# Kernel tuning notes

Measured on AMD Instinct MI355X. Metric: run time of the kernel, lower is better.

## Reference

```python
import jax, jax.numpy as jnp
import numpy as np

SCALE = 0.125  # (dim // heads) ** -0.5 = (256 // 4) ** -0.5


def setup_inputs() -> dict:
    key = jax.random.key(0)
    k1, k2, k3, k4, k5 = jax.random.split(key, 5)
    dim, red = 256, 4
    c = dim // red  # 64
    B, H, W = 4, 64, 64
    x = jax.random.normal(k1, (B, dim, H, W), dtype=jnp.float32)
    qkv_w = jax.random.normal(k2, (3 * c, dim), dtype=jnp.float32) * 0.02
    qkv_b = jax.random.normal(k3, (3 * c,), dtype=jnp.float32) * 0.02
    proj_w = jax.random.normal(k4, (dim, c), dtype=jnp.float32) * 0.02
    proj_b = jax.random.normal(k5, (dim,), dtype=jnp.float32) * 0.02
    return {"x": x, "qkv_w": qkv_w, "qkv_b": qkv_b, "proj_w": proj_w, "proj_b": proj_b}


def reference(x, qkv_w, qkv_b, proj_w, proj_b):
    B, C, H, W = x.shape
    # 1x1 conv == channel matmul
    qkv = jnp.einsum('bchw,oc->bohw', x, qkv_w) + qkv_b[None, :, None, None]
    c = qkv.shape[1] // 3
    qkv = qkv.reshape(B, 3 * c, H * W)
    q, k, v = qkv[:, :c], qkv[:, c:2 * c], qkv[:, 2 * c:]  # [B, c, HW]
    # attn[b, n, m] = sum_c q[b,c,n] * k[b,c,m] * scale
    attn = jnp.einsum('bcn,bcm->bnm', q, k) * SCALE
    attn = jax.nn.softmax(attn, axis=-1)  # [B, HW, HW]
    # out[b, c, n] = sum_m v[b,c,m] * attn[b,n,m]   (v @ attn^T)
    out = jnp.einsum('bcm,bnm->bcn', v, attn).reshape(B, c, H, W)
    # proj 1x1 conv back to dim
    return jnp.einsum('bchw,oc->bohw', out, proj_w) + proj_b[None, :, None, None]
```

## Files before the change

### kernel.cpp

```cpp
#include <hip/hip_runtime.h>
#include <hip/hip_bf16.h>


#define N_TOK 4096
#define CDIM  64
#define DIM   256
#define NBAT  4

typedef __attribute__((ext_vector_type(8)))  short          short8;
typedef __attribute__((ext_vector_type(8)))  unsigned short ushort8_t;
typedef __attribute__((ext_vector_type(4)))  unsigned short ushort4_t;
typedef __attribute__((ext_vector_type(4)))  unsigned int   uint4_t;
typedef __attribute__((ext_vector_type(4)))  float          float4_t;
typedef __attribute__((ext_vector_type(16))) float          float16_t;

#if __has_builtin(__builtin_amdgcn_exp2f)
#define QSC  0.18033688011112042f
#define PEXP(x) __builtin_amdgcn_exp2f(x)
#else
#define QSC  0.125f
#define PEXP(x) __expf(x)
#endif

__device__ __forceinline__ unsigned short f2bf(float f) {
  unsigned int u = __builtin_bit_cast(unsigned int, f);
  u += 0x7fffu + ((u >> 16) & 1u);
  return (unsigned short)(u >> 16);
}

__device__ __forceinline__ unsigned int pkcv(float a, float b) {
  __hip_bfloat162 h = __float22bfloat162_rn(make_float2(a, b));
  unsigned int r; __builtin_memcpy(&r, &h, 4); return r;
}

__device__ __forceinline__ short8 ld8(const unsigned short* p) {
  return __builtin_bit_cast(short8, *(const ushort8_t*)p);
}

__device__ __forceinline__ short8 pack8f(float4_t a, float4_t b) {
  uint4_t u;
  u[0] = pkcv(a[0], a[1]); u[1] = pkcv(a[2], a[3]);
  u[2] = pkcv(b[0], b[1]); u[3] = pkcv(b[2], b[3]);
  return __builtin_bit_cast(short8, u);
}

__device__ __forceinline__ float16_t z16() {
  float16_t r;
#pragma unroll
  for (int i = 0; i < 16; ++i) r[i] = 0.0f;
  return r;
}

typedef __attribute__((address_space(1))) const void* gvp;
typedef __attribute__((address_space(3))) void*       lvp;
__device__ __forceinline__ void dma16(const unsigned short* g, unsigned short* l) {
  __builtin_amdgcn_global_load_lds((gvp)g, (lvp)l, 16, 0, 0);
}

#define MFMA(a, b, c) __builtin_amdgcn_mfma_f32_32x32x16_bf16((a), (b), (c), 0, 0, 0)

#define QOFF  0
#define KOFF  1048576
#define VOFF  2097152
#define WQOFF 3145728
#define BSOFF 3194880

__global__ void k_prep(const float* __restrict__ qw, const float* __restrict__ qb,
                       unsigned short* __restrict__ wqs, float* __restrict__ bs)
{
  const int g = blockIdx.x * 256 + threadIdx.x;
  {
    const int lane = g & 63, grp = g >> 6;
    const int w6 = grp >> 4, kk = grp & 15;
    const int o = w6 * 32 + (lane & 31);
    const int c = kk * 16 + (lane >> 5) * 8;
    const float sc = (o < 64) ? QSC : 1.0f;
    const float* src = qw + o * 256 + c;
    ushort8_t u;
#pragma unroll
    for (int j = 0; j < 8; ++j) u[j] = f2bf(src[j] * sc);
    *(ushort8_t*)(wqs + g * 8) = u;
  }
  if (g < 48) {
    float4_t f = *(const float4_t*)(qb + g * 4);
    float4_t o;
#pragma unroll
    for (int j = 0; j < 4; ++j) o[j] = f[j] * ((g * 4 + j) < 64 ? QSC : 1.0f);
    *(float4_t*)(bs + g * 4) = o;
  }
}

#define RS 132

__global__ __launch_bounds__(768, 3) void k_qkv(
    const float* __restrict__ x, const unsigned short* __restrict__ wqs,
    const float* __restrict__ bs, unsigned short* __restrict__ Qf,
    unsigned short* __restrict__ Kf, unsigned short* __restrict__ Vf)
{
  __shared__ unsigned int Xl[64 * RS];
  const int id = blockIdx.x;
  const int b  = (id >> 1) & 3;
  const int nt = (id & 1) | ((id >> 3) << 1);
  const int t  = threadIdx.x;
  const int n0g = nt * 64;

  if (t < 512) {
    const int n0  = (t & 15) * 4;
    const int cpb = t >> 4;
#pragma unroll
    for (int p = 0; p < 4; ++p) {
      const int cp = cpb + 32 * p, c = cp * 2;
      const float* xb = x + (((size_t)(b * DIM + c)) << 12) + n0g + n0;
      float4_t a = *(const float4_t*)xb;
      float4_t d = *(const float4_t*)(xb + 4096);
#pragma unroll
      for (int j = 0; j < 4; ++j)
        Xl[(n0 + j) * RS + cp] = pkcv(a[j], d[j]);
    }
  }

  const int w = t >> 6, lane = t & 63, l31 = lane & 31, lh = lane >> 5;
  const int ot = w >> 1, sub = w & 1;
  const int ch = nt * 2 + sub;

  const unsigned short* wrow = wqs + ((ot * 16) << 9) + lane * 8;
  short8 wf[16];
#pragma unroll
  for (int kk = 0; kk < 16; ++kk) wf[kk] = ld8(wrow + (kk << 9));

  __syncthreads();

  const unsigned int* xr = &Xl[(sub * 32 + l31) * RS + lh * 4];

  float16_t a0 = z16();
  if (ot < 4) {
#pragma unroll
    for (int kk = 0; kk < 16; ++kk) {
      short8 xf = __builtin_bit_cast(short8, *(const uint4_t*)(xr + kk * 8));
      a0 = MFMA(wf[kk], xf, a0);
    }
  } else {
#pragma unroll
    for (int kk = 0; kk < 16; ++kk) {
      short8 xf = __builtin_bit_cast(short8, *(const uint4_t*)(xr + kk * 8));
      a0 = MFMA(xf, wf[kk], a0);
    }
  }

  if (ot < 4) {
    unsigned short* dst = (ot < 2) ? Qf : Kf;
    const int w2 = ot & 1;
#pragma unroll
    for (int p = 0; p < 4; ++p) {
      const int o = ot * 32 + p * 8 + lh * 4;
      float4_t bv = *(const float4_t*)(bs + o);
      ushort4_t pk4;
#pragma unroll
      for (int q = 0; q < 4; ++q) pk4[q] = f2bf(a0[p * 4 + q] + bv[q]);
      const int kkt = w2 * 2 + (p >> 1);
      *(ushort4_t*)(dst + ((((b * 128 + ch) * 4 + kkt) << 9)
                           + (l31 + 32 * (p & 1)) * 8 + lh * 4)) = pk4;
    }
  } else {
    const int ct = ot - 4;
    const float bvs = bs[128 + ct * 32 + l31];
#pragma unroll
    for (int ks = 0; ks < 2; ++ks) {
      ushort8_t pk8;
#pragma unroll
      for (int j = 0; j < 8; ++j) pk8[j] = f2bf(a0[ks * 8 + j] + bvs);
      *(ushort8_t*)(Vf + ((((b * 128 + ch) * 4 + ct * 2 + ks) << 9)
                          + lane * 8)) = pk8;
    }
  }
}

#define OS   68
#define OLS  72
#define NACC (64 * OS + 64)

__global__ __launch_bounds__(512, 1) void k_attn(
    const unsigned short* __restrict__ Qf, const unsigned short* __restrict__ Kf,
    const unsigned short* __restrict__ Vf, const float* __restrict__ pw,
    const float* __restrict__ pb, float* __restrict__ out)
{
  __shared__ __align__(16) unsigned short KV[2][2][16384];
  __shared__ float Oacc[NACC];
  __shared__ __align__(16) unsigned short Ol[64 * OLS];

  const int id = blockIdx.x;
  const int b  = (id >> 1) & 3;
  const int nt = (id & 1) | ((id >> 3) << 1);
  const int t  = threadIdx.x;
  const int wv = t >> 6, lane = t & 63, l31 = lane & 31, lh = lane >> 5;
  const int mq = wv >> 1, nsub = wv & 1;

  for (int i = t; i < NACC; i += 512) Oacc[i] = 0.0f;

  const int kvsel = wv >> 2;
  const int wq2   = (wv & 3) * 2;
  const unsigned short* sg = ((kvsel == 0) ? Kf : Vf)
                             + (((size_t)(b * 128 + wq2)) << 11) + lane * 8;

  short8 qf[4];
#pragma unroll
  for (int kk = 0; kk < 4; ++kk)
    qf[kk] = ld8(Qf + (((b * 128 + nt * 2 + nsub) * 4 + kk) << 9) + lane * 8);

#pragma unroll
  for (int c2 = 0; c2 < 2; ++c2)
#pragma unroll
    for (int kk = 0; kk < 4; ++kk)
      dma16(sg + (c2 << 11) + (kk << 9),
            &KV[0][kvsel][((wq2 + c2) << 11) + (kk << 9)]);

  float16_t oc0 = z16(), oc1 = z16();
  float den = 0.0f;

  __syncthreads();

  for (int t4 = 0; t4 < 16; ++t4) {
    const int cur = t4 & 1;

    if (t4 < 15) {
      const unsigned short* g = sg + (((size_t)(t4 + 1)) << 14);
#pragma unroll
      for (int c2 = 0; c2 < 2; ++c2)
#pragma unroll
        for (int kk = 0; kk < 4; ++kk)
          dma16(g + (c2 << 11) + (kk << 9),
                &KV[cur ^ 1][kvsel][((wq2 + c2) << 11) + (kk << 9)]);
    }

#pragma unroll
    for (int cc = 0; cc < 2; ++cc) {
      const int ch = mq * 2 + cc;
      const unsigned short* kl = &KV[cur][0][ch << 11];
      const unsigned short* vl = &KV[cur][1][ch << 11];

      short8 kf0 = ld8(kl + lane * 8);
      short8 kf1 = ld8(kl + 512 + lane * 8);
      short8 kf2 = ld8(kl + 1024 + lane * 8);
      short8 kf3 = ld8(kl + 1536 + lane * 8);

      float16_t s = z16();
      s = MFMA(kf0, qf[0], s);
      s = MFMA(kf1, qf[1], s);
      s = MFMA(kf2, qf[2], s);
      s = MFMA(kf3, qf[3], s);

      float p[16];
#pragma unroll
      for (int e = 0; e < 16; ++e) p[e] = PEXP(s[e]);
      {
        float d0 = (p[0] + p[1]) + (p[2] + p[3]);
        float d1 = (p[4] + p[5]) + (p[6] + p[7]);
        float d2 = (p[8] + p[9]) + (p[10] + p[11]);
        float d3 = (p[12] + p[13]) + (p[14] + p[15]);
        den += (d0 + d1) + (d2 + d3);
      }

      uint4_t w0, w1;
#pragma unroll
      for (int j = 0; j < 4; ++j) {
        w0[j] = pkcv(p[2 * j], p[2 * j + 1]);
        w1[j] = pkcv(p[8 + 2 * j], p[9 + 2 * j]);
      }
      short8 pf0 = __builtin_bit_cast(short8, w0);
      short8 pf1 = __builtin_bit_cast(short8, w1);

      short8 vf0 = ld8(vl + lane * 8);
      short8 vf1 = ld8(vl + 512 + lane * 8);
      short8 vf2 = ld8(vl + 1024 + lane * 8);
      short8 vf3 = ld8(vl + 1536 + lane * 8);

      oc0 = MFMA(pf0, vf0, oc0);
      oc0 = MFMA(pf1, vf1, oc0);
      oc1 = MFMA(pf0, vf2, oc1);
      oc1 = MFMA(pf1, vf3, oc1);
    }

    __syncthreads();
  }

  den += __shfl_xor(den, 32);

#pragma unroll
  for (int ct = 0; ct < 2; ++ct) {
    const float16_t& oa = ct ? oc1 : oc0;
    const int cc = ct * 32 + l31;
#pragma unroll
    for (int e = 0; e < 16; ++e) {
      const int nr = nsub * 32 + (e & 3) + 8 * (e >> 2) + 4 * lh;
      atomicAdd(&Oacc[nr * OS + cc], oa[e]);
    }
  }
  if (lane < 32) atomicAdd(&Oacc[64 * OS + nsub * 32 + l31], den);
  __syncthreads();

  {
    const int nloc = t >> 3, c8 = (t & 7) * 8;
    float4_t s0 = *(float4_t*)&Oacc[nloc * OS + c8];
    float4_t s1 = *(float4_t*)&Oacc[nloc * OS + c8 + 4];
    const float r = 1.0f / Oacc[64 * OS + nloc];
    uint4_t o4;
    o4[0] = pkcv(s0[0] * r, s0[1] * r);
    o4[1] = pkcv(s0[2] * r, s0[3] * r);
    o4[2] = pkcv(s1[0] * r, s1[1] * r);
    o4[3] = pkcv(s1[2] * r, s1[3] * r);
    *(uint4_t*)&Ol[nloc * OLS + c8] = o4;
  }
  __syncthreads();

  float16_t f0 = z16(), f1 = z16();
  const float* pwrow = pw + (wv * 32 + l31) * 64 + lh * 8;
#pragma unroll
  for (int kk = 0; kk < 4; ++kk) {
    float4_t wa = *(const float4_t*)(pwrow + kk * 16);
    float4_t wb = *(const float4_t*)(pwrow + kk * 16 + 4);
    short8 af = pack8f(wa, wb);
    short8 b0 = ld8(&Ol[l31 * OLS + kk * 16 + lh * 8]);
    short8 b1 = ld8(&Ol[(32 + l31) * OLS + kk * 16 + lh * 8]);
    f0 = MFMA(af, b0, f0);
    f1 = MFMA(af, b1, f1);
  }
  const int n0 = nt * 64;
#pragma unroll
  for (int e = 0; e < 16; ++e) {
    const int o = wv * 32 + (e & 3) + 8 * (e >> 2) + 4 * lh;
    const float bv = pb[o];
    out[((b * 256 + o) << 12) + n0 + l31]      = f0[e] + bv;
    out[((b * 256 + o) << 12) + n0 + 32 + l31] = f1[e] + bv;
  }
}

extern "C" void kernel_launch(void* const* d_in, const int* in_sizes, int n_in,
                              void* d_out, int out_size, void* d_ws, size_t ws_size,
                              hipStream_t stream) {
  const float* x      = (const float*)d_in[0];
  const float* qkv_w  = (const float*)d_in[1];
  const float* qkv_b  = (const float*)d_in[2];
  const float* proj_w = (const float*)d_in[3];
  const float* proj_b = (const float*)d_in[4];
  float* out = (float*)d_out;

  unsigned short* ws  = (unsigned short*)d_ws;
  unsigned short* qf  = ws + QOFF;
  unsigned short* kf  = ws + KOFF;
  unsigned short* vf  = ws + VOFF;
  unsigned short* wqs = ws + WQOFF;
  float*          bs  = (float*)(ws + BSOFF);

  k_prep<<<24, 256, 0, stream>>>(qkv_w, qkv_b, wqs, bs);
  k_qkv<<<256, 768, 0, stream>>>(x, wqs, bs, qf, kf, vf);
  k_attn<<<256, 512, 0, stream>>>(qf, kf, vf, proj_w, proj_b, out);
}
```

Measured before the change: 132.8 us.

## Stage only K in LDS and read V fragments directly from global memory

The shared-memory staging buffer now holds only K tiles, using the freed space to double the tile per iteration (16 chunks instead of 8, 8 iterations instead of 16). V fragments are loaded per wave straight from global memory (L2/cache) inside the inner loop rather than being DMA'd into LDS. This halves barrier count and LDS traffic for V, but puts global-load latency on the critical path right before the PV MFMAs, and each V chunk is re-read by several waves.

Result: no change. 131.0 us (-1.4%).

```diff
diff --git a/kernel.cpp b/kernel.cpp
--- a/kernel.cpp
+++ b/kernel.cpp
@@ -184,7 +184,7 @@
     const unsigned short* __restrict__ Vf, const float* __restrict__ pw,
     const float* __restrict__ pb, float* __restrict__ out)
 {
-  __shared__ __align__(16) unsigned short KV[2][2][16384];
+  __shared__ __align__(16) unsigned short Kl[2][32768];
   __shared__ float Oacc[NACC];
   __shared__ __align__(16) unsigned short Ol[64 * OLS];
 
@@ -197,46 +197,45 @@
 
   for (int i = t; i < NACC; i += 512) Oacc[i] = 0.0f;
 
-  const int kvsel = wv >> 2;
-  const int wq2   = (wv & 3) * 2;
-  const unsigned short* sg = ((kvsel == 0) ? Kf : Vf)
-                             + (((size_t)(b * 128 + wq2)) << 11) + lane * 8;
+  const int wq2 = wv * 2;
+  const unsigned short* sg = Kf + (((size_t)(b * 128 + wq2)) << 11) + lane * 8;
 
   short8 qf[4];
 #pragma unroll
   for (int kk = 0; kk < 4; ++kk)
     qf[kk] = ld8(Qf + (((b * 128 + nt * 2 + nsub) * 4 + kk) << 9) + lane * 8);
 
+  const unsigned short* vbase = Vf + (((size_t)(b * 128)) << 11) + lane * 8;
+
 #pragma unroll
   for (int c2 = 0; c2 < 2; ++c2)
 #pragma unroll
     for (int kk = 0; kk < 4; ++kk)
       dma16(sg + (c2 << 11) + (kk << 9),
-            &KV[0][kvsel][((wq2 + c2) << 11) + (kk << 9)]);
+            &Kl[0][((wq2 + c2) << 11) + (kk << 9)]);
 
   float16_t oc0 = z16(), oc1 = z16();
   float den = 0.0f;
 
   __syncthreads();
 
-  for (int t4 = 0; t4 < 16; ++t4) {
-    const int cur = t4 & 1;
-
-    if (t4 < 15) {
-      const unsigned short* g = sg + (((size_t)(t4 + 1)) << 14);
+  for (int t8 = 0; t8 < 8; ++t8) {
+    const int cur = t8 & 1;
+
+    if (t8 < 7) {
+      const unsigned short* g = sg + (((size_t)(t8 + 1)) << 15);
 #pragma unroll
       for (int c2 = 0; c2 < 2; ++c2)
 #pragma unroll
         for (int kk = 0; kk < 4; ++kk)
           dma16(g + (c2 << 11) + (kk << 9),
-                &KV[cur ^ 1][kvsel][((wq2 + c2) << 11) + (kk << 9)]);
-    }
-
-#pragma unroll
-    for (int cc = 0; cc < 2; ++cc) {
-      const int ch = mq * 2 + cc;
-      const unsigned short* kl = &KV[cur][0][ch << 11];
-      const unsigned short* vl = &KV[cur][1][ch << 11];
+                &Kl[cur ^ 1][((wq2 + c2) << 11) + (kk << 9)]);
+    }
+
+#pragma unroll
+    for (int cc = 0; cc < 4; ++cc) {
+      const int ch = mq * 4 + cc;
+      const unsigned short* kl = &Kl[cur][ch << 11];
 
       short8 kf0 = ld8(kl + lane * 8);
       short8 kf1 = ld8(kl + 512 + lane * 8);
@@ -269,10 +268,11 @@
       short8 pf0 = __builtin_bit_cast(short8, w0);
       short8 pf1 = __builtin_bit_cast(short8, w1);
 
-      short8 vf0 = ld8(vl + lane * 8);
-      short8 vf1 = ld8(vl + 512 + lane * 8);
-      short8 vf2 = ld8(vl + 1024 + lane * 8);
-      short8 vf3 = ld8(vl + 1536 + lane * 8);
+      const unsigned short* vl = vbase + (((size_t)(t8 * 16 + ch)) << 11);
+      short8 vf0 = ld8(vl);
+      short8 vf1 = ld8(vl + 512);
+      short8 vf2 = ld8(vl + 1024);
+      short8 vf3 = ld8(vl + 1536);
 
       oc0 = MFMA(pf0, vf0, oc0);
       oc0 = MFMA(pf1, vf1, oc0);
```

## Give each attention block 256 queries so each wave covers all keys

Applied to the files above, without the earlier changes.

The attention kernel is restructured so each of its 8 waves owns its own 32 query rows and loops over all keys itself. This removes the shared-memory atomic reduction of partial outputs and denominators, and the accumulator buffers that went with it. Each block now handles 256 queries, so the grid shrinks from 256 blocks to 64, and K/V tiles loaded into shared memory are reused across four times as many queries. The cost is far less parallelism: only 64 workgroups run on a GPU with many more compute units, and each wave does eight times longer inner loops.

Result: slower. 147.8 us (+11.3%).

```diff
diff --git a/kernel.cpp b/kernel.cpp
--- a/kernel.cpp
+++ b/kernel.cpp
@@ -175,9 +175,7 @@
   }
 }
 
-#define OS   68
 #define OLS  72
-#define NACC (64 * OS + 64)
 
 __global__ __launch_bounds__(512, 1) void k_attn(
     const unsigned short* __restrict__ Qf, const unsigned short* __restrict__ Kf,
@@ -185,58 +183,51 @@
     const float* __restrict__ pb, float* __restrict__ out)
 {
   __shared__ __align__(16) unsigned short KV[2][2][16384];
-  __shared__ float Oacc[NACC];
-  __shared__ __align__(16) unsigned short Ol[64 * OLS];
 
   const int id = blockIdx.x;
   const int b  = (id >> 1) & 3;
-  const int nt = (id & 1) | ((id >> 3) << 1);
+  const int qt = (id & 1) | ((id >> 3) << 1);
   const int t  = threadIdx.x;
   const int wv = t >> 6, lane = t & 63, l31 = lane & 31, lh = lane >> 5;
-  const int mq = wv >> 1, nsub = wv & 1;
-
-  for (int i = t; i < NACC; i += 512) Oacc[i] = 0.0f;
-
-  const int kvsel = wv >> 2;
-  const int wq2   = (wv & 3) * 2;
-  const unsigned short* sg = ((kvsel == 0) ? Kf : Vf)
-                             + (((size_t)(b * 128 + wq2)) << 11) + lane * 8;
-
+
+  const int cq = qt * 8 + wv;
   short8 qf[4];
 #pragma unroll
   for (int kk = 0; kk < 4; ++kk)
-    qf[kk] = ld8(Qf + (((b * 128 + nt * 2 + nsub) * 4 + kk) << 9) + lane * 8);
-
-#pragma unroll
-  for (int c2 = 0; c2 < 2; ++c2)
-#pragma unroll
-    for (int kk = 0; kk < 4; ++kk)
-      dma16(sg + (c2 << 11) + (kk << 9),
-            &KV[0][kvsel][((wq2 + c2) << 11) + (kk << 9)]);
+    qf[kk] = ld8(Qf + (((b * 128 + cq) * 4 + kk) << 9) + lane * 8);
+
+  const unsigned short* sgK = Kf + (((size_t)(b * 128 + wv)) << 11) + lane * 8;
+  const unsigned short* sgV = Vf + (((size_t)(b * 128 + wv)) << 11) + lane * 8;
+
+#pragma unroll
+  for (int kk = 0; kk < 4; ++kk)
+    dma16(sgK + (kk << 9), &KV[0][0][(wv << 11) + (kk << 9)]);
+#pragma unroll
+  for (int kk = 0; kk < 4; ++kk)
+    dma16(sgV + (kk << 9), &KV[0][1][(wv << 11) + (kk << 9)]);
 
   float16_t oc0 = z16(), oc1 = z16();
   float den = 0.0f;
 
   __syncthreads();
 
-  for (int t4 = 0; t4 < 16; ++t4) {
-    const int cur = t4 & 1;
-
-    if (t4 < 15) {
-      const unsigned short* g = sg + (((size_t)(t4 + 1)) << 14);
-#pragma unroll
-      for (int c2 = 0; c2 < 2; ++c2)
-#pragma unroll
-        for (int kk = 0; kk < 4; ++kk)
-          dma16(g + (c2 << 11) + (kk << 9),
-                &KV[cur ^ 1][kvsel][((wq2 + c2) << 11) + (kk << 9)]);
-    }
-
-#pragma unroll
-    for (int cc = 0; cc < 2; ++cc) {
-      const int ch = mq * 2 + cc;
-      const unsigned short* kl = &KV[cur][0][ch << 11];
-      const unsigned short* vl = &KV[cur][1][ch << 11];
+  for (int t16 = 0; t16 < 16; ++t16) {
+    const int cur = t16 & 1;
+
+    if (t16 < 15) {
+      const size_t go = ((size_t)(t16 + 1)) << 14;
+#pragma unroll
+      for (int kk = 0; kk < 4; ++kk)
+        dma16(sgK + go + (kk << 9), &KV[cur ^ 1][0][(wv << 11) + (kk << 9)]);
+#pragma unroll
+      for (int kk = 0; kk < 4; ++kk)
+        dma16(sgV + go + (kk << 9), &KV[cur ^ 1][1][(wv << 11) + (kk << 9)]);
+    }
+
+#pragma unroll
+    for (int cc = 0; cc < 8; ++cc) {
+      const unsigned short* kl = &KV[cur][0][cc << 11];
+      const unsigned short* vl = &KV[cur][1][cc << 11];
 
       short8 kf0 = ld8(kl + lane * 8);
       short8 kf1 = ld8(kl + 512 + lane * 8);
@@ -284,53 +275,45 @@
   }
 
   den += __shfl_xor(den, 32);
-
-#pragma unroll
-  for (int ct = 0; ct < 2; ++ct) {
-    const float16_t& oa = ct ? oc1 : oc0;
-    const int cc = ct * 32 + l31;
-#pragma unroll
-    for (int e = 0; e < 16; ++e) {
-      const int nr = nsub * 32 + (e & 3) + 8 * (e >> 2) + 4 * lh;
-      atomicAdd(&Oacc[nr * OS + cc], oa[e]);
-    }
-  }
-  if (lane < 32) atomicAdd(&Oacc[64 * OS + nsub * 32 + l31], den);
+  const float inv = 1.0f / den;
+
+  unsigned short* Ol = &KV[0][0][0];
+#pragma unroll
+  for (int e = 0; e < 16; ++e) {
+    const int r = (e & 3) + 8 * (e >> 2) + 4 * lh;
+    const float rv = __shfl(inv, r);
+    Ol[(wv * 32 + r) * OLS + l31]      = f2bf(oc0[e] * rv);
+    Ol[(wv * 32 + r) * OLS + 32 + l31] = f2bf(oc1[e] * rv);
+  }
   __syncthreads();
 
-  {
-    const int nloc = t >> 3, c8 = (t & 7) * 8;
-    float4_t s0 = *(float4_t*)&Oacc[nloc * OS + c8];
-    float4_t s1 = *(float4_t*)&Oacc[nloc * OS + c8 + 4];
-    const float r = 1.0f / Oacc[64 * OS + nloc];
-    uint4_t o4;
-    o4[0] = pkcv(s0[0] * r, s0[1] * r);
-    o4[1] = pkcv(s0[2] * r, s0[3] * r);
-    o4[2] = pkcv(s1[0] * r, s1[1] * r);
-    o4[3] = pkcv(s1[2] * r, s1[3] * r);
-    *(uint4_t*)&Ol[nloc * OLS + c8] = o4;
-  }
-  __syncthreads();
-
-  float16_t f0 = z16(), f1 = z16();
   const float* pwrow = pw + (wv * 32 + l31) * 64 + lh * 8;
+  short8 af[4];
 #pragma unroll
   for (int kk = 0; kk < 4; ++kk) {
     float4_t wa = *(const float4_t*)(pwrow + kk * 16);
     float4_t wb = *(const float4_t*)(pwrow + kk * 16 + 4);
-    short8 af = pack8f(wa, wb);
-    short8 b0 = ld8(&Ol[l31 * OLS + kk * 16 + lh * 8]);
-    short8 b1 = ld8(&Ol[(32 + l31) * OLS + kk * 16 + lh * 8]);
-    f0 = MFMA(af, b0, f0);
-    f1 = MFMA(af, b1, f1);
-  }
-  const int n0 = nt * 64;
-#pragma unroll
-  for (int e = 0; e < 16; ++e) {
-    const int o = wv * 32 + (e & 3) + 8 * (e >> 2) + 4 * lh;
-    const float bv = pb[o];
-    out[((b * 256 + o) << 12) + n0 + l31]      = f0[e] + bv;
-    out[((b * 256 + o) << 12) + n0 + 32 + l31] = f1[e] + bv;
+    af[kk] = pack8f(wa, wb);
+  }
+  float bv[16];
+#pragma unroll
+  for (int e = 0; e < 16; ++e)
+    bv[e] = pb[wv * 32 + (e & 3) + 8 * (e >> 2) + 4 * lh];
+
+  const int n0 = qt * 256;
+#pragma unroll
+  for (int ns = 0; ns < 8; ++ns) {
+    float16_t f = z16();
+#pragma unroll
+    for (int kk = 0; kk < 4; ++kk) {
+      short8 bfr = ld8(&Ol[(ns * 32 + l31) * OLS + kk * 16 + lh * 8]);
+      f = MFMA(af[kk], bfr, f);
+    }
+#pragma unroll
+    for (int e = 0; e < 16; ++e) {
+      const int o = wv * 32 + (e & 3) + 8 * (e >> 2) + 4 * lh;
+      out[((b * 256 + o) << 12) + n0 + ns * 32 + l31] = f[e] + bv[e];
+    }
   }
 }
 
@@ -353,5 +336,5 @@
 
   k_prep<<<24, 256, 0, stream>>>(qkv_w, qkv_b, wqs, bs);
   k_qkv<<<256, 768, 0, stream>>>(x, wqs, bs, qf, kf, vf);
-  k_attn<<<256, 512, 0, stream>>>(qf, kf, vf, proj_w, proj_b, out);
-}
+  k_attn<<<64, 512, 0, stream>>>(qf, kf, vf, proj_w, proj_b, out);
+}
```
